# Performance work log

Measured on AMD Instinct MI355X. Metric: run time of the kernel, lower is better.

The kernel has to match this reference:

```python
import jax, jax.numpy as jnp
import numpy as np

TOPK = 13
ALPHA = 1.0
BETA = 6.0
NUM_CLASSES = 80
NUM_ANCHORS = 100000
NUM_GT = 512
EPS = 1e-9


def _make_boxes(key, n):
    k1, k2 = jax.random.split(key)
    lt = jax.random.uniform(k1, (n, 2)) * 0.5          # x1, y1 in [0, 0.5)
    wh = jax.random.uniform(k2, (n, 2)) * 0.5 + 1e-3   # positive width/height
    return jnp.concatenate([lt, lt + wh], axis=-1)      # [n, 4] valid xyxy


def setup_inputs() -> dict:
    key = jax.random.key(0)
    k1, k2, k3, k4 = jax.random.split(key, 4)
    pd_scores = jax.random.uniform(k1, (NUM_ANCHORS, NUM_CLASSES), dtype=jnp.float32)
    pd_bboxes = _make_boxes(k2, NUM_ANCHORS)
    gt_labels = jax.random.randint(k3, (NUM_GT, 1), 0, NUM_CLASSES, dtype=jnp.int64)
    gt_bboxes = _make_boxes(k4, NUM_GT)
    return {"pd_scores": pd_scores, "pd_bboxes": pd_bboxes,
            "gt_labels": gt_labels, "gt_bboxes": gt_bboxes}


def box_iou(a, b):
    # a: [G, 4], b: [A, 4] in xyxy -> iou [G, A]
    lt = jnp.maximum(a[:, None, :2], b[None, :, :2])
    rb = jnp.minimum(a[:, None, 2:], b[None, :, 2:])
    wh = jnp.clip(rb - lt, 0.0)
    inter = wh[..., 0] * wh[..., 1]                      # [G, A]
    area_a = (a[:, 2] - a[:, 0]) * (a[:, 3] - a[:, 1])   # [G]
    area_b = (b[:, 2] - b[:, 0]) * (b[:, 3] - b[:, 1])   # [A]
    union = area_a[:, None] + area_b[None, :] - inter
    return inter / (union + EPS)


def select_topk_candidates(metrics, topk):
    # metrics: [G, A] -> bool mask [G, A] of per-row topk entries
    _, topk_idx = jax.lax.top_k(metrics, topk)           # [G, topk]
    rows = jnp.arange(metrics.shape[0])[:, None]
    mask = jnp.zeros(metrics.shape, dtype=bool)
    return mask.at[rows, topk_idx].set(True)


def reference(pd_scores, pd_bboxes, gt_labels, gt_bboxes):
    labels = gt_labels.reshape(-1)                       # [G]
    ious = box_iou(gt_bboxes, pd_bboxes)                 # [G, A]
    scores = pd_scores[:, labels].T                      # [G, A] gather by gt class
    metrics = (scores ** ALPHA) * (ious ** BETA)         # alignment metric [G, A]
    is_in_topk = select_topk_candidates(metrics, TOPK)   # [G, A] bool
    max_metrics = jnp.max(metrics, axis=0)               # [A]
    max_indices = jnp.argmax(metrics, axis=0)            # [A]
    target_labels = labels[max_indices]                  # [A]
    target_labels = jnp.where(max_metrics <= 0, NUM_CLASSES, target_labels)
    target_bboxes = gt_bboxes[max_indices]               # [A, 4]
    # is_in_topk is computed (as in the original) and returned so the topk/scatter
    return target_labels, target_bboxes, max_metrics, is_in_topk
```

## Files before the change

kernel.cpp:

```cpp
#include <hip/hip_runtime.h>
#include <cfloat>
#include <cstdint>

#define AN 100000
#define GN 512
#define NC 80
#define KK 13

#define CHUNKS 16
#define CH_LEN 6400
#define DUMP 16
#define GSLICE 8
#define GPS (GN / GSLICE)

typedef unsigned long long ull;

__device__ __forceinline__ float iou6_f(float4 g, float ga, float4 p)
{
    float pa = (p.z - p.x) * (p.w - p.y);
    float ltx = fmaxf(g.x, p.x), lty = fmaxf(g.y, p.y);
    float rbx = fminf(g.z, p.z), rby = fminf(g.w, p.w);
    float w = fmaxf(rbx - ltx, 0.0f), h = fmaxf(rby - lty, 0.0f);
    float inter = w * h;
    float uni = ga + pa - inter;
    float iou = inter / (uni + 1e-9f);
    float i2 = iou * iou;
    return i2 * i2 * i2;
}

__device__ __forceinline__ unsigned f2ord(float f)
{
    unsigned b = __float_as_uint(f);
    return b ^ (unsigned)(((int)b >> 31) | 0x80000000);
}
__device__ __forceinline__ float ord2f(unsigned u)
{
    unsigned b = (u & 0x80000000u) ? (u ^ 0x80000000u) : ~u;
    return __uint_as_float(b);
}

__device__ __forceinline__ void csw(float& va, int& ia, float& vb, int& ib)
{
    bool sw = (va < vb) || (va == vb && ia > ib);
    float tv = sw ? vb : va; int ti = sw ? ib : ia;
    vb = sw ? va : vb; ib = sw ? ia : ib;
    va = tv; ia = ti;
}

__device__ __forceinline__ void wsync()
{
    __builtin_amdgcn_sched_barrier(0);
    asm volatile("s_waitcnt lgkmcnt(0)" ::: "memory");
    __builtin_amdgcn_sched_barrier(0);
}

__device__ float flush_x(int lane, int n, const float* cand_v, const int* cand_i,
                         float& inc_v, int& inc_i)
{
    wsync();
    float v[8]; int ix[8];
    #pragma unroll
    for (int k = 0; k < 8; ++k) {
        int j = lane + (k << 6);
        bool ok = j < n;
        v[k]  = ok ? cand_v[j] : -FLT_MAX;
        ix[k] = ok ? cand_i[j] : 0x7fffffff;
    }
    csw(v[0],ix[0],v[1],ix[1]); csw(v[2],ix[2],v[3],ix[3]);
    csw(v[4],ix[4],v[5],ix[5]); csw(v[6],ix[6],v[7],ix[7]);
    csw(v[0],ix[0],v[2],ix[2]); csw(v[1],ix[1],v[3],ix[3]);
    csw(v[4],ix[4],v[6],ix[6]); csw(v[5],ix[5],v[7],ix[7]);
    csw(v[1],ix[1],v[2],ix[2]); csw(v[5],ix[5],v[6],ix[6]);
    csw(v[0],ix[0],v[4],ix[4]); csw(v[1],ix[1],v[5],ix[5]);
    csw(v[2],ix[2],v[6],ix[6]); csw(v[3],ix[3],v[7],ix[7]);
    csw(v[2],ix[2],v[4],ix[4]); csw(v[3],ix[3],v[5],ix[5]);
    csw(v[1],ix[1],v[2],ix[2]); csw(v[3],ix[3],v[4],ix[4]);
    csw(v[5],ix[5],v[6],ix[6]);
    bool c[8];
    #pragma unroll
    for (int j = 0; j < 8; ++j)
        c[j] = (v[j] > inc_v) || (v[j] == inc_v && ix[j] < inc_i);
    float h[9]; int hi[9];
    h[0] = c[0] ? v[0] : inc_v;  hi[0] = c[0] ? ix[0] : inc_i;
    #pragma unroll
    for (int j = 1; j < 8; ++j) {
        h[j]  = c[j] ? v[j]  : (c[j-1] ? inc_v : v[j-1]);
        hi[j] = c[j] ? ix[j] : (c[j-1] ? inc_i : ix[j-1]);
    }
    h[8] = c[7] ? inc_v : v[7];  hi[8] = c[7] ? inc_i : ix[7];

    float th = -FLT_MAX;
    #pragma unroll
    for (int r = 0; r < KK; ++r) {
        ull myp = ((ull)f2ord(h[0]) << 32) | (unsigned)(~hi[0]);
        ull p = myp;
        #pragma unroll
        for (int o = 32; o >= 1; o >>= 1) {
            ull q = __shfl_xor(p, o);
            p = p > q ? p : q;
        }
        float wv = ord2f((unsigned)(p >> 32));
        int   wi = (int)~((unsigned)p);
        if (lane == r) { inc_v = wv; inc_i = wi; }
        bool pop = (myp == p);
        #pragma unroll
        for (int j = 0; j < 8; ++j) {
            h[j]  = pop ? h[j+1]  : h[j];
            hi[j] = pop ? hi[j+1] : hi[j];
        }
        h[8]  = pop ? -FLT_MAX   : h[8];
        hi[8] = pop ? 0x7fffffff : hi[8];
        th = wv;
    }
    return th;
}

__device__ __forceinline__ void insert13(float* v, int* ix, float m, int a)
{
    bool worse = (m < v[KK - 1]) || (m == v[KK - 1] && a > ix[KK - 1]);
    if (worse) return;
    int p = 0;
    #pragma unroll
    for (int j = 0; j < KK; ++j)
        p += ((v[j] > m) || (v[j] == m && ix[j] < a)) ? 1 : 0;
    #pragma unroll
    for (int j = KK - 1; j >= 1; --j) {
        bool sh = (j > p);
        v[j]  = sh ? v[j - 1]  : v[j];
        ix[j] = sh ? ix[j - 1] : ix[j];
    }
    #pragma unroll
    for (int j = 0; j < KK; ++j) if (j == p) { v[j] = m; ix[j] = a; }
}

__global__ __launch_bounds__(256) void transpose_scores(
    const float* __restrict__ ps, float* __restrict__ scT)
{
    __shared__ float tile[64][NC + 1];
    int a0 = blockIdx.x * 64;
    int tid = threadIdx.x;
    for (int i = tid; i < 64 * NC / 4; i += 256) {
        int fi = i * 4;
        int a = fi / NC, c = fi % NC;
        if (a0 + a < AN) {
            float4 v = *reinterpret_cast<const float4*>(ps + (size_t)(a0 + a) * NC + c);
            tile[a][c] = v.x; tile[a][c + 1] = v.y; tile[a][c + 2] = v.z; tile[a][c + 3] = v.w;
        }
    }
    __syncthreads();
    int j = tid & 63, cg = tid >> 6;
    int a = a0 + j;
    if (a < AN) {
        for (int c = cg; c < NC; c += 4)
            scT[(size_t)c * AN + a] = tile[j][c];
    }
}

__global__ __launch_bounds__(256) void argmax_part(
    const float* __restrict__ pd_bboxes,
    const int*   __restrict__ gt_labels,
    const float* __restrict__ gt_bboxes,
    const float* __restrict__ scT,
    ull* __restrict__ part)
{
    __shared__ float4 gb[GPS];
    __shared__ float  ga[GPS];
    __shared__ int    glb[GPS];
    int slice = blockIdx.x & (GSLICE - 1);
    int ab = (blockIdx.x >> 3) * 512;
    int tid = threadIdx.x;
    int g0 = slice * GPS;
    if (tid < GPS) {
        float4 bb = ((const float4*)gt_bboxes)[g0 + tid];
        gb[tid] = bb;
        ga[tid] = (bb.z - bb.x) * (bb.w - bb.y);
        glb[tid] = gt_labels[g0 + tid];
    }
    __syncthreads();
    int aa = ab + tid, ab2 = ab + 256 + tid;
    bool okA = aa < AN, okB = ab2 < AN;
    int ca = okA ? aa : AN - 1, cb = okB ? ab2 : AN - 1;
    float4 pba = ((const float4*)pd_bboxes)[ca];
    float4 pbb = ((const float4*)pd_bboxes)[cb];
    float bestA = -1.0f, bestB = -1.0f;
    int bgA = 0, bgB = 0;
    for (int i = 0; i < GPS; ++i) {
        float4 gx = gb[i];
        float gax = ga[i];
        int lab = glb[i];
        const float* srow = scT + (size_t)lab * AN;
        float i6a = iou6_f(gx, gax, pba);
        float i6b = iou6_f(gx, gax, pbb);
        float sa = (i6a > bestA) ? srow[ca] : 0.0f;
        float sb = (i6b > bestB) ? srow[cb] : 0.0f;
        float ma = sa * i6a;
        float mb = sb * i6b;
        if (ma > bestA) { bestA = ma; bgA = i; }
        if (mb > bestB) { bestB = mb; bgB = i; }
    }
    if (okA)
        part[(size_t)slice * AN + aa] =
            ((ull)__float_as_uint(bestA) << 32) | (ull)(0xFFFFFFFFu - (unsigned)(g0 + bgA));
    if (okB)
        part[(size_t)slice * AN + ab2] =
            ((ull)__float_as_uint(bestB) << 32) | (ull)(0xFFFFFFFFu - (unsigned)(g0 + bgB));
}

__global__ __launch_bounds__(256) void argmax_combine(
    const ull* __restrict__ part,
    const int* __restrict__ gt_labels,
    const float* __restrict__ gt_bboxes,
    float* __restrict__ out)
{
    int a = blockIdx.x * 256 + threadIdx.x;
    if (a >= AN) return;
    ull p = part[a];
    #pragma unroll
    for (int s = 1; s < GSLICE; ++s) {
        ull q = part[(size_t)s * AN + a];
        p = p > q ? p : q;
    }
    unsigned g = 0xFFFFFFFFu - (unsigned)(p & 0xFFFFFFFFull);
    float best = __uint_as_float((unsigned)(p >> 32));
    out[a] = (best <= 0.0f) ? (float)NC : (float)gt_labels[g];
    ((float4*)(out + AN))[a] = ((const float4*)gt_bboxes)[g];
    out[(size_t)5 * AN + a] = best;
}

template<bool FULL>
__device__ __forceinline__ void tile256(
    int tb, int aend, int lane, uint64_t lt,
    const float4* __restrict__ pd4, const float* __restrict__ srow,
    float4 b, float gax, float& th, int& cnt,
    float* cand_v, int* cand_i, float& inc_v, int& inc_i)
{
    int a0 = tb + lane, a1 = a0 + 64, a2 = a0 + 128, a3 = a0 + 192;
    int c0 = FULL ? a0 : min(a0, AN - 1);
    int c1 = FULL ? a1 : min(a1, AN - 1);
    int c2 = FULL ? a2 : min(a2, AN - 1);
    int c3 = FULL ? a3 : min(a3, AN - 1);
    float4 B0 = pd4[c0], B1 = pd4[c1], B2 = pd4[c2], B3 = pd4[c3];
    float i60 = iou6_f(b, gax, B0);
    float i61 = iou6_f(b, gax, B1);
    float i62 = iou6_f(b, gax, B2);
    float i63 = iou6_f(b, gax, B3);
    bool h0 = (i60 > th) && (FULL || a0 < aend);
    bool h1 = (i61 > th) && (FULL || a1 < aend);
    bool h2 = (i62 > th) && (FULL || a2 < aend);
    bool h3 = (i63 > th) && (FULL || a3 < aend);
    if (__any(h0 | h1 | h2 | h3)) {
        float s0 = h0 ? srow[c0] : 0.0f;
        float s1 = h1 ? srow[c1] : 0.0f;
        float s2 = h2 ? srow[c2] : 0.0f;
        float s3 = h3 ? srow[c3] : 0.0f;
        float m0 = s0 * i60, m1 = s1 * i61, m2 = s2 * i62, m3 = s3 * i63;
        h0 = h0 && (m0 > th); h1 = h1 && (m1 > th);
        h2 = h2 && (m2 > th); h3 = h3 && (m3 > th);
        uint64_t B;
        B = __ballot(h0);
        if (h0) { int p = cnt + __popcll(B & lt); cand_v[p] = m0; cand_i[p] = a0; }
        cnt += __popcll(B);
        B = __ballot(h1);
        if (h1) { int p = cnt + __popcll(B & lt); cand_v[p] = m1; cand_i[p] = a1; }
        cnt += __popcll(B);
        B = __ballot(h2);
        if (h2) { int p = cnt + __popcll(B & lt); cand_v[p] = m2; cand_i[p] = a2; }
        cnt += __popcll(B);
        B = __ballot(h3);
        if (h3) { int p = cnt + __popcll(B & lt); cand_v[p] = m3; cand_i[p] = a3; }
        cnt += __popcll(B);
        if (cnt >= 256) {
            th = flush_x(lane, cnt, cand_v, cand_i, inc_v, inc_i);
            cnt = 0;
        }
    }
}

__global__ __launch_bounds__(256, 4) void topk_pass1(
    const float* __restrict__ pd_bboxes,
    const int*   __restrict__ gt_labels,
    const float* __restrict__ gt_bboxes,
    const float* __restrict__ scT,
    float* __restrict__ out_v, int* __restrict__ out_i)
{
    __shared__ float cvA[4][512];
    __shared__ int   ciA[4][512];
    int w = threadIdx.x >> 6, lane = threadIdx.x & 63;
    float* cand_v = cvA[w]; int* cand_i = ciA[w];
    uint64_t lt = (1ull << lane) - 1ull;
    int gid = blockIdx.x * 4 + w;
    int g = gid & (GN - 1), c = gid >> 9;

    float4 b = ((const float4*)gt_bboxes)[g];
    float gax = (b.z - b.x) * (b.w - b.y);
    int lab = gt_labels[g];
    const float* srow = scT + (size_t)lab * AN;
    const float4* pd4 = (const float4*)pd_bboxes;

    int base = c * CH_LEN;
    int len = min(CH_LEN, AN - base);
    int nfull = len >> 8, rem = len & 255;
    int aend = base + len;

    float th = -FLT_MAX; int cnt = 0;
    float inc_v = -FLT_MAX; int inc_i = 0x7fffffff;

    for (int it = 0; it < nfull; ++it)
        tile256<true>(base + (it << 8), aend, lane, lt, pd4, srow,
                      b, gax, th, cnt, cand_v, cand_i, inc_v, inc_i);
    if (rem)
        tile256<false>(base + (nfull << 8), aend, lane, lt, pd4, srow,
                       b, gax, th, cnt, cand_v, cand_i, inc_v, inc_i);

    if (cnt > 0)
        flush_x(lane, cnt, cand_v, cand_i, inc_v, inc_i);

    if (lane < DUMP) {
        size_t o = ((size_t)g * CHUNKS + c) * DUMP + lane;
        out_v[o] = (lane < KK) ? inc_v : -FLT_MAX;
        out_i[o] = (lane < KK) ? inc_i : 0x7fffffff;
    }
}

__global__ __launch_bounds__(256) void topk_finalize(
    const float* __restrict__ in_v, const int* __restrict__ in_i,
    float* __restrict__ mask)
{
    int g = blockIdx.x, tid = threadIdx.x;
    float4* row4 = (float4*)(mask + (size_t)g * AN);
    float4 z = make_float4(0.f, 0.f, 0.f, 0.f);
    for (int j = tid; j < AN / 4; j += 256) row4[j] = z;
    __syncthreads();
    if (tid >= 64) return;
    int lane = tid;
    size_t rb = (size_t)g * (CHUNKS * DUMP);
    float v0 = in_v[rb + lane],       v1 = in_v[rb + 64 + lane];
    float v2 = in_v[rb + 128 + lane], v3 = in_v[rb + 192 + lane];
    int   i0 = in_i[rb + lane],       i1 = in_i[rb + 64 + lane];
    int   i2 = in_i[rb + 128 + lane], i3 = in_i[rb + 192 + lane];
    csw(v0, i0, v1, i1); csw(v2, i2, v3, i3);
    csw(v0, i0, v2, i2); csw(v1, i1, v3, i3);
    csw(v1, i1, v2, i2);
    #pragma unroll
    for (int r = 0; r < KK; ++r) {
        ull myp = ((ull)f2ord(v0) << 32) | (unsigned)(~i0);
        ull p = myp;
        #pragma unroll
        for (int o = 32; o >= 1; o >>= 1) {
            ull q = __shfl_xor(p, o);
            p = p > q ? p : q;
        }
        int wi = (int)~((unsigned)p);
        if (lane == r) mask[(size_t)g * AN + wi] = 1.0f;
        bool pop = (myp == p);
        v0 = pop ? v1 : v0;  i0 = pop ? i1 : i0;
        v1 = pop ? v2 : v1;  i1 = pop ? i2 : i1;
        v2 = pop ? v3 : v2;  i2 = pop ? i3 : i2;
        v3 = pop ? -FLT_MAX : v3;  i3 = pop ? 0x7fffffff : i3;
    }
}

__global__ __launch_bounds__(256) void argmax_kernel(
    const float* __restrict__ pd_scores,
    const float* __restrict__ pd_bboxes,
    const int*   __restrict__ gt_labels,
    const float* __restrict__ gt_bboxes,
    const float* __restrict__ scT, int use_t,
    float* __restrict__ out)
{
    __shared__ float4 gb[GN];
    __shared__ float  ga[GN];
    __shared__ int    gl[GN];
    int tid = threadIdx.x;
    for (int g = tid; g < GN; g += 256) {
        float4 b = reinterpret_cast<const float4*>(gt_bboxes)[g];
        gb[g] = b;
        ga[g] = (b.z - b.x) * (b.w - b.y);
        gl[g] = gt_labels[g];
    }
    __syncthreads();
    int a = blockIdx.x * 256 + tid;
    if (a >= AN) return;
    float4 pb = reinterpret_cast<const float4*>(pd_bboxes)[a];
    float best = -1.0f; int bg = 0;
    for (int g = 0; g < GN; ++g) {
        int lab = gl[g];
        float sc = use_t ? scT[(size_t)lab * AN + a] : pd_scores[(size_t)a * NC + lab];
        float m = sc * iou6_f(gb[g], ga[g], pb);
        if (m > best) { best = m; bg = g; }
    }
    out[a] = (best <= 0.0f) ? (float)NC : (float)gl[bg];
    reinterpret_cast<float4*>(out + AN)[a] = gb[bg];
    out[5 * AN + a] = best;
}

__global__ __launch_bounds__(256) void topk_kernel_fallback(
    const float* __restrict__ pd_scores,
    const float* __restrict__ pd_bboxes,
    const int*   __restrict__ gt_labels,
    const float* __restrict__ gt_bboxes,
    const float* __restrict__ scT, int use_t,
    float* __restrict__ mask)
{
    __shared__ float sv[256 * KK];
    __shared__ int   si[256 * KK];
    int g = blockIdx.x, tid = threadIdx.x;
    float4 b = reinterpret_cast<const float4*>(gt_bboxes)[g];
    float gax = (b.z - b.x) * (b.w - b.y);
    int lab = gt_labels[g];
    float v[KK]; int idx[KK];
    #pragma unroll
    for (int j = 0; j < KK; ++j) { v[j] = -FLT_MAX; idx[j] = 0x7fffffff; }
    for (int a = tid; a < AN; a += 256) {
        float4 pb = reinterpret_cast<const float4*>(pd_bboxes)[a];
        float sc = use_t ? scT[(size_t)lab * AN + a] : pd_scores[(size_t)a * NC + lab];
        float m = sc * iou6_f(b, gax, pb);
        insert13(v, idx, m, a);
    }
    #pragma unroll
    for (int j = 0; j < KK; ++j) { sv[tid * KK + j] = v[j]; si[tid * KK + j] = idx[j]; }
    for (int off = 128; off >= 1; off >>= 1) {
        __syncthreads();
        if (tid < off) {
            int i = 0, jj = 0;
            float ov[KK]; int oi[KK];
            #pragma unroll
            for (int t = 0; t < KK; ++t) {
                float va = sv[tid * KK + i];          int ia = si[tid * KK + i];
                float vb = sv[(tid + off) * KK + jj]; int ib = si[(tid + off) * KK + jj];
                bool ta = (va > vb) || (va == vb && ia < ib);
                ov[t] = ta ? va : vb; oi[t] = ta ? ia : ib;
                i += ta ? 1 : 0; jj += ta ? 0 : 1;
            }
            #pragma unroll
            for (int t = 0; t < KK; ++t) { sv[tid * KK + t] = ov[t]; si[tid * KK + t] = oi[t]; }
        }
    }
    __syncthreads();
    if (tid < KK) mask[(size_t)g * AN + si[tid]] = 1.0f;
}

extern "C" void kernel_launch(void* const* d_in, const int* in_sizes, int n_in,
                              void* d_out, int out_size, void* d_ws, size_t ws_size,
                              hipStream_t stream)
{
    const float* pd_scores = (const float*)d_in[0];
    const float* pd_bboxes = (const float*)d_in[1];
    const int*   gt_labels = (const int*)d_in[2];
    const float* gt_bboxes = (const float*)d_in[3];
    float* out  = (float*)d_out;
    float* mask = out + (size_t)6 * AN;

    const size_t scT_b  = (size_t)NC * AN * sizeof(float);
    const size_t auxn   = (size_t)GN * CHUNKS * DUMP;
    const size_t aux_b  = auxn * 8;
    const size_t part_b = (size_t)GSLICE * AN * sizeof(ull);

    float* scT   = (float*)d_ws;
    float* aux_v = (float*)((char*)d_ws + scT_b);
    int*   aux_i = (int*)(aux_v + auxn);
    ull*   part  = (ull*)((char*)d_ws + scT_b + aux_b);

    if (ws_size >= scT_b + aux_b + part_b) {
        transpose_scores<<<(AN + 63) / 64, 256, 0, stream>>>(pd_scores, scT);
        topk_pass1<<<GN * CHUNKS / 4, 256, 0, stream>>>(
            pd_bboxes, gt_labels, gt_bboxes, scT, aux_v, aux_i);
        topk_finalize<<<GN, 256, 0, stream>>>(aux_v, aux_i, mask);
        argmax_part<<<((AN + 511) / 512) * GSLICE, 256, 0, stream>>>(
            pd_bboxes, gt_labels, gt_bboxes, scT, part);
        argmax_combine<<<(AN + 255) / 256, 256, 0, stream>>>(
            part, gt_labels, gt_bboxes, out);
    } else if (ws_size >= scT_b + aux_b) {
        transpose_scores<<<(AN + 63) / 64, 256, 0, stream>>>(pd_scores, scT);
        topk_pass1<<<GN * CHUNKS / 4, 256, 0, stream>>>(
            pd_bboxes, gt_labels, gt_bboxes, scT, aux_v, aux_i);
        topk_finalize<<<GN, 256, 0, stream>>>(aux_v, aux_i, mask);
        argmax_kernel<<<(AN + 255) / 256, 256, 0, stream>>>(
            pd_scores, pd_bboxes, gt_labels, gt_bboxes, scT, 1, out);
    } else if (ws_size >= scT_b) {
        hipMemsetAsync(mask, 0, (size_t)GN * AN * sizeof(float), stream);
        transpose_scores<<<(AN + 63) / 64, 256, 0, stream>>>(pd_scores, scT);
        argmax_kernel<<<(AN + 255) / 256, 256, 0, stream>>>(
            pd_scores, pd_bboxes, gt_labels, gt_bboxes, scT, 1, out);
        topk_kernel_fallback<<<GN, 256, 0, stream>>>(
            pd_scores, pd_bboxes, gt_labels, gt_bboxes, scT, 1, mask);
    } else {
        hipMemsetAsync(mask, 0, (size_t)GN * AN * sizeof(float), stream);
        argmax_kernel<<<(AN + 255) / 256, 256, 0, stream>>>(
            pd_scores, pd_bboxes, gt_labels, gt_bboxes, scT, 0, out);
        topk_kernel_fallback<<<GN, 256, 0, stream>>>(
            pd_scores, pd_bboxes, gt_labels, gt_bboxes, scT, 0, mask);
    }
}
```

Baseline: 213.7 us.

## Double-buffer topk tile loads, load scores unconditionally, halve chunk count

Each top-k scan wave now prefetches the next 256-anchor tile of boxes and class scores into registers while it processes the current tile, ping-ponging between two register sets. Scores are loaded for every anchor instead of only those passing the IoU threshold pre-filter. The anchor range is split into 8 chunks instead of 16, so the finalize kernel merges 2 candidates per lane instead of 4. This trades more register pressure, extra score-row bandwidth and fewer scan waves (less parallelism) for hiding load latency and a cheaper merge.

```diff
diff --git a/kernel.cpp b/kernel.cpp
--- a/kernel.cpp
+++ b/kernel.cpp
@@ -7,8 +7,8 @@
 #define NC 80
 #define KK 13
 
-#define CHUNKS 16
-#define CH_LEN 6400
+#define CHUNKS 8
+#define CH_LEN 12544
 #define DUMP 16
 #define GSLICE 8
 #define GPS (GN / GSLICE)
@@ -227,35 +227,37 @@
     out[(size_t)5 * AN + a] = best;
 }
 
-template<bool FULL>
-__device__ __forceinline__ void tile256(
+__device__ __forceinline__ void loadT(int tb, int lane,
+    const float4* __restrict__ pd4, const float* __restrict__ srow,
+    float4& B0, float4& B1, float4& B2, float4& B3,
+    float& s0, float& s1, float& s2, float& s3)
+{
+    int a0 = tb + lane;
+    int c0 = min(a0,       AN - 1);
+    int c1 = min(a0 + 64,  AN - 1);
+    int c2 = min(a0 + 128, AN - 1);
+    int c3 = min(a0 + 192, AN - 1);
+    B0 = pd4[c0]; B1 = pd4[c1]; B2 = pd4[c2]; B3 = pd4[c3];
+    s0 = srow[c0]; s1 = srow[c1]; s2 = srow[c2]; s3 = srow[c3];
+}
+
+__device__ __forceinline__ void procT(
     int tb, int aend, int lane, uint64_t lt,
-    const float4* __restrict__ pd4, const float* __restrict__ srow,
+    float4 B0, float4 B1, float4 B2, float4 B3,
+    float s0, float s1, float s2, float s3,
     float4 b, float gax, float& th, int& cnt,
     float* cand_v, int* cand_i, float& inc_v, int& inc_i)
 {
     int a0 = tb + lane, a1 = a0 + 64, a2 = a0 + 128, a3 = a0 + 192;
-    int c0 = FULL ? a0 : min(a0, AN - 1);
-    int c1 = FULL ? a1 : min(a1, AN - 1);
-    int c2 = FULL ? a2 : min(a2, AN - 1);
-    int c3 = FULL ? a3 : min(a3, AN - 1);
-    float4 B0 = pd4[c0], B1 = pd4[c1], B2 = pd4[c2], B3 = pd4[c3];
-    float i60 = iou6_f(b, gax, B0);
-    float i61 = iou6_f(b, gax, B1);
-    float i62 = iou6_f(b, gax, B2);
-    float i63 = iou6_f(b, gax, B3);
-    bool h0 = (i60 > th) && (FULL || a0 < aend);
-    bool h1 = (i61 > th) && (FULL || a1 < aend);
-    bool h2 = (i62 > th) && (FULL || a2 < aend);
-    bool h3 = (i63 > th) && (FULL || a3 < aend);
+    float m0 = s0 * iou6_f(b, gax, B0);
+    float m1 = s1 * iou6_f(b, gax, B1);
+    float m2 = s2 * iou6_f(b, gax, B2);
+    float m3 = s3 * iou6_f(b, gax, B3);
+    bool h0 = (m0 > th) && (a0 < aend);
+    bool h1 = (m1 > th) && (a1 < aend);
+    bool h2 = (m2 > th) && (a2 < aend);
+    bool h3 = (m3 > th) && (a3 < aend);
     if (__any(h0 | h1 | h2 | h3)) {
-        float s0 = h0 ? srow[c0] : 0.0f;
-        float s1 = h1 ? srow[c1] : 0.0f;
-        float s2 = h2 ? srow[c2] : 0.0f;
-        float s3 = h3 ? srow[c3] : 0.0f;
-        float m0 = s0 * i60, m1 = s1 * i61, m2 = s2 * i62, m3 = s3 * i63;
-        h0 = h0 && (m0 > th); h1 = h1 && (m1 > th);
-        h2 = h2 && (m2 > th); h3 = h3 && (m3 > th);
         uint64_t B;
         B = __ballot(h0);
         if (h0) { int p = cnt + __popcll(B & lt); cand_v[p] = m0; cand_i[p] = a0; }
@@ -299,18 +301,31 @@
 
     int base = c * CH_LEN;
     int len = min(CH_LEN, AN - base);
-    int nfull = len >> 8, rem = len & 255;
     int aend = base + len;
+    int NT = (len + 255) >> 8;
 
     float th = -FLT_MAX; int cnt = 0;
     float inc_v = -FLT_MAX; int inc_i = 0x7fffffff;
 
-    for (int it = 0; it < nfull; ++it)
-        tile256<true>(base + (it << 8), aend, lane, lt, pd4, srow,
-                      b, gax, th, cnt, cand_v, cand_i, inc_v, inc_i);
-    if (rem)
-        tile256<false>(base + (nfull << 8), aend, lane, lt, pd4, srow,
-                       b, gax, th, cnt, cand_v, cand_i, inc_v, inc_i);
+    float4 X0, X1, X2, X3, Y0, Y1, Y2, Y3;
+    float xs0, xs1, xs2, xs3, ys0, ys1, ys2, ys3;
+
+    loadT(base, lane, pd4, srow, X0, X1, X2, X3, xs0, xs1, xs2, xs3);
+    int i = 0, tb = base;
+    while (true) {
+        if (i + 1 < NT)
+            loadT(tb + 256, lane, pd4, srow, Y0, Y1, Y2, Y3, ys0, ys1, ys2, ys3);
+        procT(tb, aend, lane, lt, X0, X1, X2, X3, xs0, xs1, xs2, xs3,
+              b, gax, th, cnt, cand_v, cand_i, inc_v, inc_i);
+        ++i; tb += 256;
+        if (i >= NT) break;
+        if (i + 1 < NT)
+            loadT(tb + 256, lane, pd4, srow, X0, X1, X2, X3, xs0, xs1, xs2, xs3);
+        procT(tb, aend, lane, lt, Y0, Y1, Y2, Y3, ys0, ys1, ys2, ys3,
+              b, gax, th, cnt, cand_v, cand_i, inc_v, inc_i);
+        ++i; tb += 256;
+        if (i >= NT) break;
+    }
 
     if (cnt > 0)
         flush_x(lane, cnt, cand_v, cand_i, inc_v, inc_i);
@@ -334,13 +349,9 @@
     if (tid >= 64) return;
     int lane = tid;
     size_t rb = (size_t)g * (CHUNKS * DUMP);
-    float v0 = in_v[rb + lane],       v1 = in_v[rb + 64 + lane];
-    float v2 = in_v[rb + 128 + lane], v3 = in_v[rb + 192 + lane];
-    int   i0 = in_i[rb + lane],       i1 = in_i[rb + 64 + lane];
-    int   i2 = in_i[rb + 128 + lane], i3 = in_i[rb + 192 + lane];
-    csw(v0, i0, v1, i1); csw(v2, i2, v3, i3);
-    csw(v0, i0, v2, i2); csw(v1, i1, v3, i3);
-    csw(v1, i1, v2, i2);
+    float v0 = in_v[rb + lane], v1 = in_v[rb + 64 + lane];
+    int   i0 = in_i[rb + lane], i1 = in_i[rb + 64 + lane];
+    csw(v0, i0, v1, i1);
     #pragma unroll
     for (int r = 0; r < KK; ++r) {
         ull myp = ((ull)f2ord(v0) << 32) | (unsigned)(~i0);
@@ -353,10 +364,8 @@
         int wi = (int)~((unsigned)p);
         if (lane == r) mask[(size_t)g * AN + wi] = 1.0f;
         bool pop = (myp == p);
-        v0 = pop ? v1 : v0;  i0 = pop ? i1 : i0;
-        v1 = pop ? v2 : v1;  i1 = pop ? i2 : i1;
-        v2 = pop ? v3 : v2;  i2 = pop ? i3 : i2;
-        v3 = pop ? -FLT_MAX : v3;  i3 = pop ? 0x7fffffff : i3;
+        v0 = pop ? v1 : v0;          i0 = pop ? i1 : i0;
+        v1 = pop ? -FLT_MAX : v1;    i1 = pop ? 0x7fffffff : i1;
     }
 }
 
```

Result: faster. 205.8 us (-3.7%).
